# Kernel tuning notes

Hardware: AMD Instinct MI355X
Metric: run time of the kernel (lower is better)

The kernel has to match this reference:

```python
import jax, jax.numpy as jnp
import numpy as np


def mesa_head(xh, yh, qh, lam):
    # xh = per-head 'inputs' (v_proj output), yh = 'targets' (k_proj output),
    # qh = queries; all [T, d]. lam is this head's scalar lambda.
    T, d = xh.shape
    init_inv = jnp.eye(d, dtype=xh.dtype) * lam

    def step(inv, tok):
        x_t, q_t = tok
        Hx = inv @ x_t                      # [d]   (cur_inverse @ x)
        xH = x_t @ inv                      # [d]   (x^T @ cur_inverse)
        denom = 1.0 + x_t @ Hx              # scalar: forward=1 + x^T H x
        new_inv = inv - jnp.outer(Hx, xH) / denom   # Sherman-Morrison rank-1 update
        return new_inv, new_inv @ q_t       # pred_t = S_t @ q_t

    _, preds = jax.lax.scan(step, init_inv, (xh, qh))  # preds: [T, d]

    # scaled_dot_product_attention(preds, xh, yh) with masked=True,
    # use_softmax=False, normalization=False: tril-masked linear attention.
    logits = preds @ xh.T                               # [T, T]
    mask = jnp.tril(jnp.ones((T, T), dtype=bool))
    logits = jnp.where(mask, logits, jnp.zeros((), dtype=logits.dtype))
    return logits @ yh                                  # [T, d]


def reference(x, Wq, Wk, Wv, Wo, lambdas):
    B, T, E = x.shape
    H = lambdas.shape[0]
    d = Wq.shape[1] // H
    q = (x @ Wq).reshape(B, T, H, d)   # query_heads
    k = (x @ Wk).reshape(B, T, H, d)   # target_heads
    v = (x @ Wv).reshape(B, T, H, d)   # input_heads
    # Original call: mesa(input_heads, target_heads, query_heads, lambdas, norm)
    over_batch = jax.vmap(mesa_head, in_axes=(0, 0, 0, None))
    over_heads = jax.vmap(over_batch, in_axes=(2, 2, 2, 0), out_axes=-1)
    mesa_out = over_heads(v, k, q, lambdas)             # [B, T, d, H]
    # Faithful to original: reshape combines (d, H) in that order before o_proj.
    out = mesa_out.reshape(B, T, H * d) @ Wo            # [B, T, E]
    return out


def setup_inputs() -> dict:
    key = jax.random.key(0)
    ks = jax.random.split(key, 6)
    B, T, E, H, d = 2, 1024, 512, 8, 64
    s_in = 1.0 / np.sqrt(E).astype(np.float32)
    s_out = 1.0 / np.sqrt(H * d).astype(np.float32)
    return {
        "x": jax.random.normal(ks[0], (B, T, E), dtype=jnp.float32),
        "Wq": jax.random.normal(ks[1], (E, H * d), dtype=jnp.float32) * s_in,
        "Wk": jax.random.normal(ks[2], (E, H * d), dtype=jnp.float32) * s_in,
        "Wv": jax.random.normal(ks[3], (E, H * d), dtype=jnp.float32) * s_in,
        "Wo": jax.random.normal(ks[4], (H * d, E), dtype=jnp.float32) * s_out,
        "lambdas": jnp.ones((H,), dtype=jnp.float32),
    }
```

## Files before the change

### kernel.cpp

```cpp
#include <hip/hip_runtime.h>

#define T_SEQ 1024
#define DH 64
#define NH 8
#define NB 2
#define EMB 512
#define CS 32
#define NCH 32
#define ACH 16
#define NCHAIN 16

typedef __attribute__((ext_vector_type(8))) short bf16x8;
typedef __attribute__((ext_vector_type(4))) float f32x4;

__device__ __forceinline__ int swz4(int r, int c4) {
    return r * 16 + ((c4 ^ (r >> 2)) & 15);
}

__device__ __forceinline__ void fma4(float4& o, float s, const float4& b) {
    o.x += s * b.x; o.y += s * b.y; o.z += s * b.z; o.w += s * b.w;
}

__device__ __forceinline__ ushort f2bf(float f) {
    unsigned u = __float_as_uint(f);
    return (ushort)((u + 0x7FFFu + ((u >> 16) & 1u)) >> 16);
}
__device__ __forceinline__ float bf2f(ushort h) {
    return __uint_as_float(((unsigned)h) << 16);
}
__device__ __forceinline__ void split2(float f, ushort& hi, ushort& lo) {
    hi = f2bf(f);
    lo = f2bf(f - bf2f(hi));
}

__global__ __launch_bounds__(256) void prep_qkv(
    const float* __restrict__ x, const float* __restrict__ W0,
    const float* __restrict__ W1, const float* __restrict__ W2,
    ushort* __restrict__ x_hi, ushort* __restrict__ x_lo,
    ushort* __restrict__ Wt_hi, ushort* __restrict__ Wt_lo) {
    int zz = blockIdx.z;
    int t = threadIdx.x;
    __shared__ float T[64][65];
    if (zz < 3) {
        const float* W = (zz == 0) ? W0 : (zz == 1) ? W1 : W2;
        ushort* hi = Wt_hi + (size_t)zz * 262144;
        ushort* lo = Wt_lo + (size_t)zz * 262144;
        int kk0 = blockIdx.x * 64, n0 = blockIdx.y * 64;
#pragma unroll
        for (int i = 0; i < 4; ++i) {
            int rl = i * 16 + (t >> 4);
            float4 vv = *(const float4*)&W[(size_t)(kk0 + rl) * 512 + n0 + (t & 15) * 4];
            T[rl][(t & 15) * 4 + 0] = vv.x;
            T[rl][(t & 15) * 4 + 1] = vv.y;
            T[rl][(t & 15) * 4 + 2] = vv.z;
            T[rl][(t & 15) * 4 + 3] = vv.w;
        }
        __syncthreads();
        int nl = t >> 2, kl = (t & 3) * 16;
#pragma unroll
        for (int j4 = 0; j4 < 4; ++j4) {
            ushort4 h4, l4;
            split2(T[kl + j4 * 4 + 0][nl], h4.x, l4.x);
            split2(T[kl + j4 * 4 + 1][nl], h4.y, l4.y);
            split2(T[kl + j4 * 4 + 2][nl], h4.z, l4.z);
            split2(T[kl + j4 * 4 + 3][nl], h4.w, l4.w);
            size_t dst = (size_t)(n0 + nl) * 512 + kk0 + kl + j4 * 4;
            *(ushort4*)&hi[dst] = h4;
            *(ushort4*)&lo[dst] = l4;
        }
    } else {
        int bid = blockIdx.y * 8 + blockIdx.x;
        const float4* in = (const float4*)x;
        ushort4* hi = (ushort4*)x_hi;
        ushort4* lo = (ushort4*)x_lo;
#pragma unroll
        for (int i = 0; i < 16; ++i) {
            int id = (bid * 16 + i) * 256 + t;
            float4 xv = in[id];
            ushort4 h, l;
            split2(xv.x, h.x, l.x);
            split2(xv.y, h.y, l.y);
            split2(xv.z, h.z, l.z);
            split2(xv.w, h.w, l.w);
            hi[id] = h;
            lo[id] = l;
        }
    }
}

template <int MODE>
__global__ __launch_bounds__(256) void mfma_gemm(
    const ushort* __restrict__ Ahi, const ushort* __restrict__ Alo,
    const ushort* __restrict__ Bth, const ushort* __restrict__ Btl,
    float* __restrict__ o0, float* __restrict__ o1, float* __restrict__ o2) {
    int bm = blockIdx.x, bn = blockIdx.y, zz = blockIdx.z;
    const ushort* Bh = Bth + (size_t)zz * 262144;
    const ushort* Bl = Btl + (size_t)zz * 262144;
    float* out = (MODE == 0) ? ((zz == 0) ? o0 : (zz == 1) ? o1 : o2) : o0;

    __shared__ ushort Ash[128 * 40];
    __shared__ ushort Asl[128 * 40];
    __shared__ ushort Bsh[64 * 40];
    __shared__ ushort Bsl[64 * 40];

    int tid = threadIdx.x;
    int lane = tid & 63, wid = tid >> 6;
    int wm = wid >> 1, wn = wid & 1;
    int fr = lane & 15, fk = (lane >> 4) * 8;
    int sr = tid >> 2, sc = (tid & 3) * 8;

    f32x4 zero = {0.f, 0.f, 0.f, 0.f};
    f32x4 acc[4][2];
#pragma unroll
    for (int f = 0; f < 4; ++f)
#pragma unroll
        for (int g = 0; g < 2; ++g) acc[f][g] = zero;

    const ushort* gAh = Ahi + (size_t)(bm * 128 + sr) * 512 + sc;
    const ushort* gAl = Alo + (size_t)(bm * 128 + sr) * 512 + sc;
    const ushort* gBh = Bh + (size_t)(bn * 64 + sr) * 512 + sc;
    const ushort* gBl = Bl + (size_t)(bn * 64 + sr) * 512 + sc;

    for (int k0 = 0; k0 < 512; k0 += 32) {
        uint4 a0 = *(const uint4*)(gAh + k0);
        uint4 a1 = *(const uint4*)(gAh + 64 * 512 + k0);
        uint4 a2 = *(const uint4*)(gAl + k0);
        uint4 a3 = *(const uint4*)(gAl + 64 * 512 + k0);
        uint4 b0 = *(const uint4*)(gBh + k0);
        uint4 b1 = *(const uint4*)(gBl + k0);
        __syncthreads();
        *(uint4*)&Ash[sr * 40 + sc] = a0;
        *(uint4*)&Ash[(sr + 64) * 40 + sc] = a1;
        *(uint4*)&Asl[sr * 40 + sc] = a2;
        *(uint4*)&Asl[(sr + 64) * 40 + sc] = a3;
        *(uint4*)&Bsh[sr * 40 + sc] = b0;
        *(uint4*)&Bsl[sr * 40 + sc] = b1;
        __syncthreads();
        bf16x8 ah[4], al[4], bh[2], blo[2];
#pragma unroll
        for (int f = 0; f < 4; ++f) {
            int r = wm * 64 + f * 16 + fr;
            ah[f] = *(const bf16x8*)&Ash[r * 40 + fk];
            al[f] = *(const bf16x8*)&Asl[r * 40 + fk];
        }
#pragma unroll
        for (int g = 0; g < 2; ++g) {
            int r = wn * 32 + g * 16 + fr;
            bh[g] = *(const bf16x8*)&Bsh[r * 40 + fk];
            blo[g] = *(const bf16x8*)&Bsl[r * 40 + fk];
        }
#pragma unroll
        for (int f = 0; f < 4; ++f)
#pragma unroll
            for (int g = 0; g < 2; ++g) {
                acc[f][g] = __builtin_amdgcn_mfma_f32_16x16x32_bf16(
                    ah[f], bh[g], acc[f][g], 0, 0, 0);
                acc[f][g] = __builtin_amdgcn_mfma_f32_16x16x32_bf16(
                    ah[f], blo[g], acc[f][g], 0, 0, 0);
                acc[f][g] = __builtin_amdgcn_mfma_f32_16x16x32_bf16(
                    al[f], bh[g], acc[f][g], 0, 0, 0);
            }
    }

    int rbase = (lane >> 4) * 4;
#pragma unroll
    for (int f = 0; f < 4; ++f)
#pragma unroll
        for (int g = 0; g < 2; ++g)
#pragma unroll
            for (int j = 0; j < 4; ++j) {
                int m = bm * 128 + wm * 64 + f * 16 + rbase + j;
                int n = bn * 64 + wn * 32 + g * 16 + (lane & 15);
                float val = acc[f][g][j];
                if (MODE == 0) {
                    int b = m >> 10, tt = m & 1023;
                    int h = n >> 6, d = n & 63;
                    out[(((size_t)(b * 8 + h) * 1024 + tt) << 6) + d] = val;
                } else {
                    out[(size_t)m * 512 + n] = val;
                }
            }
}

__global__ __launch_bounds__(256) void gram_kernel(
    const float* __restrict__ v, float* __restrict__ g) {
    int chain = blockIdx.x, chunk = blockIdx.y;
    const float* X = v + ((size_t)chain * T_SEQ + chunk * CS) * DH;
    __shared__ float Xs[CS * 64];
    int tid = threadIdx.x;
#pragma unroll
    for (int i = 0; i < (CS * 16) / 256; ++i)
        ((float4*)Xs)[i * 256 + tid] = ((const float4*)X)[i * 256 + tid];
    __syncthreads();

    int tx = tid & 15, ty = tid >> 4;
    float acc[4][4];
#pragma unroll
    for (int i = 0; i < 4; ++i)
#pragma unroll
        for (int j = 0; j < 4; ++j) acc[i][j] = 0.f;

#pragma unroll 4
    for (int t = 0; t < CS; ++t) {
        float a_[4], b_[4];
#pragma unroll
        for (int i = 0; i < 4; ++i) a_[i] = Xs[t * 64 + ty * 4 + i];
#pragma unroll
        for (int j = 0; j < 4; ++j) b_[j] = Xs[t * 64 + tx * 4 + j];
#pragma unroll
        for (int i = 0; i < 4; ++i)
#pragma unroll
            for (int j = 0; j < 4; ++j) acc[i][j] += a_[i] * b_[j];
    }

    float* gp = g + ((size_t)chain * NCH + chunk) * 4096;
#pragma unroll
    for (int i = 0; i < 4; ++i)
        *(float4*)(gp + (ty * 4 + i) * 64 + tx * 4) =
            make_float4(acc[i][0], acc[i][1], acc[i][2], acc[i][3]);
}

__global__ __launch_bounds__(256) void prefix_kernel(float* __restrict__ g) {
    int gid = blockIdx.x * 256 + threadIdx.x;
    int chain = gid >> 12, elem = gid & 4095;
    float* p = g + (size_t)chain * NCH * 4096 + elem;
    float vals[NCH];
#pragma unroll
    for (int c = 0; c < NCH; ++c) vals[c] = p[(size_t)c * 4096];
    float run = 0.f;
#pragma unroll
    for (int c = 0; c < NCH; ++c) {
        float t = vals[c];
        vals[c] = run;
        run += t;
    }
#pragma unroll
    for (int c = 0; c < NCH; ++c) p[(size_t)c * 4096] = vals[c];
}

__global__ __launch_bounds__(256) void invscan(
    const float* __restrict__ g, const float* __restrict__ v,
    const float* __restrict__ q, const float* __restrict__ lambdas,
    float* __restrict__ preds) {
    int blk = blockIdx.x;
    int chain = blk >> 5, chunk = blk & 31;
    int tid = threadIdx.x;
    int row = tid >> 2, ch = tid & 3, wav = tid >> 6;
    float lam = lambdas[chain & (NH - 1)];

    __shared__ float rbuf[2][64];
    __shared__ float sbuf[2][64];
    __shared__ float Xs[CS * 64];
    __shared__ float Qs[CS * 64];
    __shared__ float Po[CS * 64];
    __shared__ float red[2][6][4];

    float m[16];
    {
        const float4* gp = (const float4*)(g + ((size_t)chain * NCH + chunk) * 4096);
#pragma unroll
        for (int i = 0; i < 4; ++i) {
            float4 t4 = gp[row * 16 + ch * 4 + i];
            m[i * 4 + 0] = t4.x; m[i * 4 + 1] = t4.y;
            m[i * 4 + 2] = t4.z; m[i * 4 + 3] = t4.w;
        }
    }
#pragma unroll
    for (int i = 0; i < 16; ++i)
        if (ch * 16 + i == row) m[i] += lam;

    const float4* vb = (const float4*)(v + ((size_t)chain * T_SEQ + chunk * CS) * DH);
    const float4* qb = (const float4*)(q + ((size_t)chain * T_SEQ + chunk * CS) * DH);
    ((float4*)Xs)[tid] = vb[tid];
    ((float4*)Xs)[256 + tid] = vb[256 + tid];
    ((float4*)Qs)[tid] = qb[tid];
    ((float4*)Qs)[256 + tid] = qb[256 + tid];

    if (row == 0) {
#pragma unroll
        for (int i = 0; i < 4; ++i)
            ((float4*)rbuf[0])[ch * 4 + i] =
                make_float4(m[i * 4], m[i * 4 + 1], m[i * 4 + 2], m[i * 4 + 3]);
    }
    if (row == 1) {
#pragma unroll
        for (int i = 0; i < 4; ++i)
            ((float4*)sbuf[0])[ch * 4 + i] =
                make_float4(m[i * 4], m[i * 4 + 1], m[i * 4 + 2], m[i * 4 + 3]);
    }
    __syncthreads();

#pragma unroll
    for (int pp = 0; pp < 32; ++pp) {
        const int p = 2 * pp;
        const float* rb = rbuf[pp & 1];
        const float* sb = sbuf[pp & 1];
        float r_[16], s_[16];
#pragma unroll
        for (int i = 0; i < 4; ++i) {
            float4 t4 = ((const float4*)rb)[ch * 4 + i];
            r_[i * 4] = t4.x; r_[i * 4 + 1] = t4.y;
            r_[i * 4 + 2] = t4.z; r_[i * 4 + 3] = t4.w;
            float4 u4 = ((const float4*)sb)[ch * 4 + i];
            s_[i * 4] = u4.x; s_[i * 4 + 1] = u4.y;
            s_[i * 4 + 2] = u4.z; s_[i * 4 + 3] = u4.w;
        }
        float rp = rb[p], rp2 = rb[p + 1], sp2 = sb[p + 1];
        float gr = rb[row], gs = sb[row];
        float i1 = 1.f / rp;
        float al = rp2 * i1;
        float i2 = 1.f / (sp2 - al * rp2);
        float c0, ca, cb;
        if (row == p) {
            c0 = 0.f; ca = i1 + al * al * i2; cb = -al * i2;
        } else if (row == p + 1) {
            c0 = 0.f; ca = -al * i2; cb = i2;
        } else {
            float b2 = (gs - al * gr) * i2;
            c0 = 1.f; ca = al * b2 - gr * i1; cb = -b2;
        }
#pragma unroll
        for (int i = 0; i < 16; ++i) m[i] = c0 * m[i] + ca * r_[i] + cb * s_[i];
        if (ch == (p >> 4)) {
            m[p & 15] = -ca;
            m[(p & 15) + 1] = -cb;
        }
        if (pp < 31) {
            if (row == p + 2) {
#pragma unroll
                for (int i = 0; i < 4; ++i)
                    ((float4*)rbuf[(pp + 1) & 1])[ch * 4 + i] =
                        make_float4(m[i * 4], m[i * 4 + 1], m[i * 4 + 2], m[i * 4 + 3]);
            }
            if (row == p + 3) {
#pragma unroll
                for (int i = 0; i < 4; ++i)
                    ((float4*)sbuf[(pp + 1) & 1])[ch * 4 + i] =
                        make_float4(m[i * 4], m[i * 4 + 1], m[i * 4 + 2], m[i * 4 + 3]);
            }
        }
        __syncthreads();
    }

#pragma unroll
    for (int tp = 0; tp < 16; ++tp) {
        const int ta = 2 * tp, tb2 = 2 * tp + 1;
        const int par = tp & 1;
        float pu = 0.f, pw = 0.f, pza = 0.f, pzb = 0.f;
#pragma unroll
        for (int i = 0; i < 4; ++i) {
            float4 xa = ((const float4*)(Xs + ta * 64))[ch * 4 + i];
            float4 xb = ((const float4*)(Xs + tb2 * 64))[ch * 4 + i];
            float4 qa = ((const float4*)(Qs + ta * 64))[ch * 4 + i];
            float4 q4 = ((const float4*)(Qs + tb2 * 64))[ch * 4 + i];
            pu += m[i * 4] * xa.x + m[i * 4 + 1] * xa.y + m[i * 4 + 2] * xa.z + m[i * 4 + 3] * xa.w;
            pw += m[i * 4] * xb.x + m[i * 4 + 1] * xb.y + m[i * 4 + 2] * xb.z + m[i * 4 + 3] * xb.w;
            pza += m[i * 4] * qa.x + m[i * 4 + 1] * qa.y + m[i * 4 + 2] * qa.z + m[i * 4 + 3] * qa.w;
            pzb += m[i * 4] * q4.x + m[i * 4 + 1] * q4.y + m[i * 4 + 2] * q4.z + m[i * 4 + 3] * q4.w;
        }
        pu += __shfl_xor(pu, 1); pu += __shfl_xor(pu, 2);
        pw += __shfl_xor(pw, 1); pw += __shfl_xor(pw, 2);
        pza += __shfl_xor(pza, 1); pza += __shfl_xor(pza, 2);
        pzb += __shfl_xor(pzb, 1); pzb += __shfl_xor(pzb, 2);
        float u = -pu, w = -pw, za = -pza, zb = -pzb;
        if (ch == 0) rbuf[par][row] = u;
        if (ch == 1) sbuf[par][row] = w;
        float a_ = Xs[ta * 64 + row], b_ = Xs[tb2 * 64 + row];
        float qa_ = Qs[ta * 64 + row], qb_ = Qs[tb2 * 64 + row];
        float d0 = a_ * u, d1 = b_ * u, d2 = b_ * w;
        float d3 = qa_ * u, d4 = qb_ * u, d5 = qb_ * w;
#pragma unroll
        for (int off = 32; off; off >>= 1) {
            d0 += __shfl_xor(d0, off); d1 += __shfl_xor(d1, off);
            d2 += __shfl_xor(d2, off); d3 += __shfl_xor(d3, off);
            d4 += __shfl_xor(d4, off); d5 += __shfl_xor(d5, off);
        }
        if ((tid & 63) == 0) {
            red[par][0][wav] = d0; red[par][1][wav] = d1; red[par][2][wav] = d2;
            red[par][3][wav] = d3; red[par][4][wav] = d4; red[par][5][wav] = d5;
        }
        __syncthreads();
        float saa = 0.25f * (red[par][0][0] + red[par][0][1] + red[par][0][2] + red[par][0][3]);
        float sab = 0.25f * (red[par][1][0] + red[par][1][1] + red[par][1][2] + red[par][1][3]);
        float sbb = 0.25f * (red[par][2][0] + red[par][2][1] + red[par][2][2] + red[par][2][3]);
        float c1  = 0.25f * (red[par][3][0] + red[par][3][1] + red[par][3][2] + red[par][3][3]);
        float c2  = 0.25f * (red[par][4][0] + red[par][4][1] + red[par][4][2] + red[par][4][3]);
        float c3  = 0.25f * (red[par][5][0] + red[par][5][1] + red[par][5][2] + red[par][5][3]);
        float k1 = 1.f / (1.f + saa);
        float al2 = sab * k1;
        float k2 = 1.f / (1.f + sbb - sab * al2);
        float vr = w - al2 * u;
        if (ch == 0) Po[ta * 64 + row] = za - (c1 * k1) * u;
        if (ch == 1) Po[tb2 * 64 + row] = zb - (c2 * k1) * u - (k2 * (c3 - al2 * c2)) * vr;
        float cu = k1 * u - al2 * k2 * vr;
        float cw = k2 * vr;
#pragma unroll
        for (int i = 0; i < 4; ++i) {
            float4 uj = ((const float4*)rbuf[par])[ch * 4 + i];
            float4 wj = ((const float4*)sbuf[par])[ch * 4 + i];
            m[i * 4 + 0] += cu * uj.x + cw * wj.x;
            m[i * 4 + 1] += cu * uj.y + cw * wj.y;
            m[i * 4 + 2] += cu * uj.z + cw * wj.z;
            m[i * 4 + 3] += cu * uj.w + cw * wj.w;
        }
    }
    __syncthreads();

    float4* po4 = (float4*)(preds + ((size_t)chain * T_SEQ + chunk * CS) * DH);
    po4[tid] = ((const float4*)Po)[tid];
    po4[256 + tid] = ((const float4*)Po)[256 + tid];
}

__global__ __launch_bounds__(256) void kvg_wot(
    const float* __restrict__ V, const float* __restrict__ Kv,
    float* __restrict__ D, const float* __restrict__ Wo,
    ushort* __restrict__ Wot_hi, ushort* __restrict__ Wot_lo) {
    __shared__ float smem[8192];
    int tid = threadIdx.x;
    if (blockIdx.y < 16) {
        int chain = blockIdx.x, ck = blockIdx.y;
        float* Vs = smem;
        float* Ks2 = smem + 4096;
        const float4* Vb = (const float4*)(V + ((size_t)chain * T_SEQ + ck * 64) * DH);
        const float4* Kb = (const float4*)(Kv + ((size_t)chain * T_SEQ + ck * 64) * DH);
#pragma unroll
        for (int i = 0; i < 4; ++i) {
            ((float4*)Vs)[i * 256 + tid] = Vb[i * 256 + tid];
            ((float4*)Ks2)[i * 256 + tid] = Kb[i * 256 + tid];
        }
        __syncthreads();

        int tx = tid & 15, ty = tid >> 4;
        float acc[4][4];
#pragma unroll
        for (int i = 0; i < 4; ++i)
#pragma unroll
            for (int j = 0; j < 4; ++j) acc[i][j] = 0.f;

#pragma unroll 4
        for (int t = 0; t < 64; ++t) {
            float a_[4], b_[4];
#pragma unroll
            for (int i = 0; i < 4; ++i) a_[i] = Vs[t * 64 + ty * 4 + i];
#pragma unroll
            for (int j = 0; j < 4; ++j) b_[j] = Ks2[t * 64 + tx * 4 + j];
#pragma unroll
            for (int i = 0; i < 4; ++i)
#pragma unroll
                for (int j = 0; j < 4; ++j) acc[i][j] += a_[i] * b_[j];
        }

        float* dp = D + ((size_t)chain * ACH + ck) * 4096;
#pragma unroll
        for (int i = 0; i < 4; ++i)
            *(float4*)(dp + (ty * 4 + i) * 64 + tx * 4) =
                make_float4(acc[i][0], acc[i][1], acc[i][2], acc[i][3]);
    } else {
        int wb = blockIdx.x * 4 + (blockIdx.y - 16);
        int kk0 = (wb >> 3) * 64, n0 = (wb & 7) * 64;
#pragma unroll
        for (int i = 0; i < 4; ++i) {
            int rl = i * 16 + (tid >> 4);
            int rs = rl * 8 + (kk0 >> 6);
            float4 vv = *(const float4*)&Wo[(size_t)rs * 512 + n0 + (tid & 15) * 4];
            smem[rl * 65 + (tid & 15) * 4 + 0] = vv.x;
            smem[rl * 65 + (tid & 15) * 4 + 1] = vv.y;
            smem[rl * 65 + (tid & 15) * 4 + 2] = vv.z;
            smem[rl * 65 + (tid & 15) * 4 + 3] = vv.w;
        }
        __syncthreads();
        int nl = tid >> 2, kl = (tid & 3) * 16;
#pragma unroll
        for (int j4 = 0; j4 < 4; ++j4) {
            ushort4 h4, l4;
            split2(smem[(kl + j4 * 4 + 0) * 65 + nl], h4.x, l4.x);
            split2(smem[(kl + j4 * 4 + 1) * 65 + nl], h4.y, l4.y);
            split2(smem[(kl + j4 * 4 + 2) * 65 + nl], h4.z, l4.z);
            split2(smem[(kl + j4 * 4 + 3) * 65 + nl], h4.w, l4.w);
            size_t dst = (size_t)(n0 + nl) * 512 + kk0 + kl + j4 * 4;
            *(ushort4*)&Wot_hi[dst] = h4;
            *(ushort4*)&Wot_lo[dst] = l4;
        }
    }
}

__global__ __launch_bounds__(256) void kv_prefix(float* __restrict__ d) {
    int gid = blockIdx.x * 256 + threadIdx.x;
    int chain = gid >> 12, elem = gid & 4095;
    float* p = d + (size_t)chain * ACH * 4096 + elem;
    float vals[ACH];
#pragma unroll
    for (int c = 0; c < ACH; ++c) vals[c] = p[(size_t)c * 4096];
    float run = 0.f;
#pragma unroll
    for (int c = 0; c < ACH; ++c) {
        float t = vals[c];
        vals[c] = run;
        run += t;
    }
#pragma unroll
    for (int c = 0; c < ACH; ++c) p[(size_t)c * 4096] = vals[c];
}

__global__ __launch_bounds__(256) void attn_chunk(
    const float* __restrict__ P, const float* __restrict__ V,
    const float* __restrict__ Kv, const float* __restrict__ C,
    ushort* __restrict__ A2_hi, ushort* __restrict__ A2_lo) {
    int ck = blockIdx.x, bh = blockIdx.y;
    int tid = threadIdx.x, tx = tid & 15, ty = tid >> 4;

    __shared__ float4 Ps[64 * 16];
    __shared__ float4 Bs[64 * 16];
    __shared__ float4 Ks[64 * 16];

    int lr = tid >> 2, lc = tid & 3;
    const float4* Pb = (const float4*)(P + ((size_t)bh * T_SEQ + ck * 64) * DH);
    const float4* Vb = (const float4*)(V + ((size_t)bh * T_SEQ + ck * 64) * DH);
    const float4* Kb = (const float4*)(Kv + ((size_t)bh * T_SEQ + ck * 64) * DH);
    const float4* Cb = (const float4*)(C + ((size_t)bh * ACH + ck) * 4096);
#pragma unroll
    for (int i = 0; i < 4; ++i) {
        Ps[swz4(lr, lc + i * 4)] = Pb[lr * 16 + lc + i * 4];
        Bs[swz4(lr, lc + i * 4)] = Cb[lr * 16 + lc + i * 4];
        Ks[swz4(lr, lc + i * 4)] = Kb[lr * 16 + lc + i * 4];
    }

    float4 o[4];
    o[0] = o[1] = o[2] = o[3] = make_float4(0.f, 0.f, 0.f, 0.f);
    __syncthreads();

    const float* Pf = (const float*)Ps;
#pragma unroll 4
    for (int j = 0; j < 64; ++j) {
        float4 b4 = Bs[swz4(j, tx)];
#pragma unroll
        for (int i = 0; i < 4; ++i) {
            float s = Pf[swz4(ty * 4 + i, j >> 2) * 4 + (j & 3)];
            fma4(o[i], s, b4);
        }
    }
    __syncthreads();

#pragma unroll
    for (int i = 0; i < 4; ++i)
        Bs[swz4(lr, lc + i * 4)] = Vb[lr * 16 + lc + i * 4];
    __syncthreads();

    float4 sa[4][4];
#pragma unroll
    for (int i = 0; i < 4; ++i)
#pragma unroll
        for (int j = 0; j < 4; ++j) sa[i][j] = make_float4(0.f, 0.f, 0.f, 0.f);
#pragma unroll
    for (int d4 = 0; d4 < 16; ++d4) {
        float4 a[4], b[4];
#pragma unroll
        for (int i = 0; i < 4; ++i) a[i] = Ps[swz4(ty * 4 + i, d4)];
#pragma unroll
        for (int j = 0; j < 4; ++j) b[j] = Bs[swz4(tx * 4 + j, d4)];
#pragma unroll
        for (int i = 0; i < 4; ++i)
#pragma unroll
            for (int j = 0; j < 4; ++j) {
                sa[i][j].x += a[i].x * b[j].x;
                sa[i][j].y += a[i].y * b[j].y;
                sa[i][j].z += a[i].z * b[j].z;
                sa[i][j].w += a[i].w * b[j].w;
            }
    }
    __syncthreads();

#pragma unroll
    for (int i = 0; i < 4; ++i) {
        int m = ty * 4 + i;
        float sv[4];
#pragma unroll
        for (int j = 0; j < 4; ++j) {
            float s = sa[i][j].x + sa[i][j].y + sa[i][j].z + sa[i][j].w;
            if ((tx * 4 + j) > m) s = 0.f;
            sv[j] = s;
        }
        Bs[swz4(m, tx)] = make_float4(sv[0], sv[1], sv[2], sv[3]);
    }
    __syncthreads();

    const float* Sf = (const float*)Bs;
#pragma unroll 4
    for (int j = 0; j < 64; ++j) {
        float4 b4 = Ks[swz4(j, tx)];
#pragma unroll
        for (int i = 0; i < 4; ++i) {
            float s = Sf[swz4(ty * 4 + i, j >> 2) * 4 + (j & 3)];
            fma4(o[i], s, b4);
        }
    }

    int kkb = ((bh & 7) << 6) + tx * 4;
#pragma unroll
    for (int i = 0; i < 4; ++i) {
        int t = ck * 64 + ty * 4 + i;
        size_t mrow = (size_t)((bh >> 3) << 10) + t;
        ushort4 h, l;
        split2(o[i].x, h.x, l.x);
        split2(o[i].y, h.y, l.y);
        split2(o[i].z, h.z, l.z);
        split2(o[i].w, h.w, l.w);
        *(ushort4*)&A2_hi[mrow * 512 + kkb] = h;
        *(ushort4*)&A2_lo[mrow * 512 + kkb] = l;
    }
}

extern "C" void kernel_launch(void* const* d_in, const int* in_sizes, int n_in,
                              void* d_out, int out_size, void* d_ws, size_t ws_size,
                              hipStream_t stream) {
    const float* x = (const float*)d_in[0];
    const float* Wq = (const float*)d_in[1];
    const float* Wk = (const float*)d_in[2];
    const float* Wv = (const float*)d_in[3];
    const float* Wo = (const float*)d_in[4];
    const float* lambdas = (const float*)d_in[5];
    float* out = (float*)d_out;

    float* ws = (float*)d_ws;
    const size_t SZ = (size_t)NB * NH * T_SEQ * DH;
    float* q = ws;
    float* k = ws + SZ;
    float* v = ws + 2 * SZ;
    float* preds = ws + 3 * SZ;
    ushort* x_hi = (ushort*)(ws + 3 * SZ);
    ushort* x_lo = (ushort*)(ws + 3 * SZ + SZ / 2);
    float* g = ws + 4 * SZ;
    ushort* Wt_hi = (ushort*)(ws + 4 * SZ);
    ushort* Wt_lo = (ushort*)(ws + 4 * SZ + 393216);
    float* dbuf = g;
    ushort* A2_hi = (ushort*)(ws + 5 * SZ);
    ushort* A2_lo = (ushort*)(ws + 5 * SZ + SZ / 2);
    ushort* Wot_hi = (ushort*)ws;
    ushort* Wot_lo = (ushort*)(ws + 131072);

    prep_qkv<<<dim3(8, 8, 4), 256, 0, stream>>>(x, Wq, Wk, Wv,
                                                x_hi, x_lo, Wt_hi, Wt_lo);
    mfma_gemm<0><<<dim3(16, 8, 3), 256, 0, stream>>>(
        x_hi, x_lo, Wt_hi, Wt_lo, q, k, v);
    gram_kernel<<<dim3(NCHAIN, NCH), 256, 0, stream>>>(v, g);
    prefix_kernel<<<dim3(256), 256, 0, stream>>>(g);
    invscan<<<dim3(NCHAIN * NCH), 256, 0, stream>>>(g, v, q, lambdas, preds);
    kvg_wot<<<dim3(NCHAIN, ACH + 4), 256, 0, stream>>>(v, k, dbuf, Wo,
                                                       Wot_hi, Wot_lo);
    kv_prefix<<<dim3(256), 256, 0, stream>>>(dbuf);
    attn_chunk<<<dim3(ACH, NCHAIN), 256, 0, stream>>>(preds, v, k, dbuf,
                                                      A2_hi, A2_lo);
    mfma_gemm<1><<<dim3(16, 8, 1), 256, 0, stream>>>(
        A2_hi, A2_lo, Wot_hi, Wot_lo, out, out, out);
}
```

Baseline: 129.0 us.

## Merge inverse scan with KV gram blocks and move Wo transpose into attention

Fuses the inverse-scan kernel and the chunked K^T V gram kernel into one launch with heterogeneous blocks. When the workspace is large enough, the KV products go to a separate buffer so they no longer alias the gram buffer. The Wo bf16 split/transpose moves from the KV kernel into the attention kernel as extra blocks. This cuts launches and lets independent work fill idle CUs alongside the long serial inverse scan, at the cost of larger shared memory per block (a fixed 8192-float array) and possible occupancy loss.

```diff
diff --git a/kernel.cpp b/kernel.cpp
--- a/kernel.cpp
+++ b/kernel.cpp
@@ -238,190 +238,192 @@
     for (int c = 0; c < NCH; ++c) p[(size_t)c * 4096] = vals[c];
 }
 
-__global__ __launch_bounds__(256) void invscan(
+__global__ __launch_bounds__(256) void invscan_kv(
+    int nInv,
     const float* __restrict__ g, const float* __restrict__ v,
     const float* __restrict__ q, const float* __restrict__ lambdas,
-    float* __restrict__ preds) {
-    int blk = blockIdx.x;
-    int chain = blk >> 5, chunk = blk & 31;
+    float* __restrict__ preds,
+    const float* __restrict__ Kv, float* __restrict__ D) {
+    __shared__ float smem[8192];
+    int bid = blockIdx.x;
     int tid = threadIdx.x;
-    int row = tid >> 2, ch = tid & 3, wav = tid >> 6;
-    float lam = lambdas[chain & (NH - 1)];
-
-    __shared__ float rbuf[2][64];
-    __shared__ float sbuf[2][64];
-    __shared__ float Xs[CS * 64];
-    __shared__ float Qs[CS * 64];
-    __shared__ float Po[CS * 64];
-    __shared__ float red[2][6][4];
-
-    float m[16];
-    {
-        const float4* gp = (const float4*)(g + ((size_t)chain * NCH + chunk) * 4096);
-#pragma unroll
-        for (int i = 0; i < 4; ++i) {
-            float4 t4 = gp[row * 16 + ch * 4 + i];
-            m[i * 4 + 0] = t4.x; m[i * 4 + 1] = t4.y;
-            m[i * 4 + 2] = t4.z; m[i * 4 + 3] = t4.w;
-        }
-    }
-#pragma unroll
-    for (int i = 0; i < 16; ++i)
-        if (ch * 16 + i == row) m[i] += lam;
-
-    const float4* vb = (const float4*)(v + ((size_t)chain * T_SEQ + chunk * CS) * DH);
-    const float4* qb = (const float4*)(q + ((size_t)chain * T_SEQ + chunk * CS) * DH);
-    ((float4*)Xs)[tid] = vb[tid];
-    ((float4*)Xs)[256 + tid] = vb[256 + tid];
-    ((float4*)Qs)[tid] = qb[tid];
-    ((float4*)Qs)[256 + tid] = qb[256 + tid];
-
-    if (row == 0) {
-#pragma unroll
-        for (int i = 0; i < 4; ++i)
-            ((float4*)rbuf[0])[ch * 4 + i] =
-                make_float4(m[i * 4], m[i * 4 + 1], m[i * 4 + 2], m[i * 4 + 3]);
-    }
-    if (row == 1) {
-#pragma unroll
-        for (int i = 0; i < 4; ++i)
-            ((float4*)sbuf[0])[ch * 4 + i] =
-                make_float4(m[i * 4], m[i * 4 + 1], m[i * 4 + 2], m[i * 4 + 3]);
-    }
-    __syncthreads();
-
-#pragma unroll
-    for (int pp = 0; pp < 32; ++pp) {
-        const int p = 2 * pp;
-        const float* rb = rbuf[pp & 1];
-        const float* sb = sbuf[pp & 1];
-        float r_[16], s_[16];
-#pragma unroll
-        for (int i = 0; i < 4; ++i) {
-            float4 t4 = ((const float4*)rb)[ch * 4 + i];
-            r_[i * 4] = t4.x; r_[i * 4 + 1] = t4.y;
-            r_[i * 4 + 2] = t4.z; r_[i * 4 + 3] = t4.w;
-            float4 u4 = ((const float4*)sb)[ch * 4 + i];
-            s_[i * 4] = u4.x; s_[i * 4 + 1] = u4.y;
-            s_[i * 4 + 2] = u4.z; s_[i * 4 + 3] = u4.w;
-        }
-        float rp = rb[p], rp2 = rb[p + 1], sp2 = sb[p + 1];
-        float gr = rb[row], gs = sb[row];
-        float i1 = 1.f / rp;
-        float al = rp2 * i1;
-        float i2 = 1.f / (sp2 - al * rp2);
-        float c0, ca, cb;
-        if (row == p) {
-            c0 = 0.f; ca = i1 + al * al * i2; cb = -al * i2;
-        } else if (row == p + 1) {
-            c0 = 0.f; ca = -al * i2; cb = i2;
-        } else {
-            float b2 = (gs - al * gr) * i2;
-            c0 = 1.f; ca = al * b2 - gr * i1; cb = -b2;
-        }
-#pragma unroll
-        for (int i = 0; i < 16; ++i) m[i] = c0 * m[i] + ca * r_[i] + cb * s_[i];
-        if (ch == (p >> 4)) {
-            m[p & 15] = -ca;
-            m[(p & 15) + 1] = -cb;
-        }
-        if (pp < 31) {
-            if (row == p + 2) {
-#pragma unroll
-                for (int i = 0; i < 4; ++i)
-                    ((float4*)rbuf[(pp + 1) & 1])[ch * 4 + i] =
-                        make_float4(m[i * 4], m[i * 4 + 1], m[i * 4 + 2], m[i * 4 + 3]);
-            }
-            if (row == p + 3) {
-#pragma unroll
-                for (int i = 0; i < 4; ++i)
-                    ((float4*)sbuf[(pp + 1) & 1])[ch * 4 + i] =
-                        make_float4(m[i * 4], m[i * 4 + 1], m[i * 4 + 2], m[i * 4 + 3]);
-            }
-        }
-        __syncthreads();
-    }
-
-#pragma unroll
-    for (int tp = 0; tp < 16; ++tp) {
-        const int ta = 2 * tp, tb2 = 2 * tp + 1;
-        const int par = tp & 1;
-        float pu = 0.f, pw = 0.f, pza = 0.f, pzb = 0.f;
-#pragma unroll
-        for (int i = 0; i < 4; ++i) {
-            float4 xa = ((const float4*)(Xs + ta * 64))[ch * 4 + i];
-            float4 xb = ((const float4*)(Xs + tb2 * 64))[ch * 4 + i];
-            float4 qa = ((const float4*)(Qs + ta * 64))[ch * 4 + i];
-            float4 q4 = ((const float4*)(Qs + tb2 * 64))[ch * 4 + i];
-            pu += m[i * 4] * xa.x + m[i * 4 + 1] * xa.y + m[i * 4 + 2] * xa.z + m[i * 4 + 3] * xa.w;
-            pw += m[i * 4] * xb.x + m[i * 4 + 1] * xb.y + m[i * 4 + 2] * xb.z + m[i * 4 + 3] * xb.w;
-            pza += m[i * 4] * qa.x + m[i * 4 + 1] * qa.y + m[i * 4 + 2] * qa.z + m[i * 4 + 3] * qa.w;
-            pzb += m[i * 4] * q4.x + m[i * 4 + 1] * q4.y + m[i * 4 + 2] * q4.z + m[i * 4 + 3] * q4.w;
-        }
-        pu += __shfl_xor(pu, 1); pu += __shfl_xor(pu, 2);
-        pw += __shfl_xor(pw, 1); pw += __shfl_xor(pw, 2);
-        pza += __shfl_xor(pza, 1); pza += __shfl_xor(pza, 2);
-        pzb += __shfl_xor(pzb, 1); pzb += __shfl_xor(pzb, 2);
-        float u = -pu, w = -pw, za = -pza, zb = -pzb;
-        if (ch == 0) rbuf[par][row] = u;
-        if (ch == 1) sbuf[par][row] = w;
-        float a_ = Xs[ta * 64 + row], b_ = Xs[tb2 * 64 + row];
-        float qa_ = Qs[ta * 64 + row], qb_ = Qs[tb2 * 64 + row];
-        float d0 = a_ * u, d1 = b_ * u, d2 = b_ * w;
-        float d3 = qa_ * u, d4 = qb_ * u, d5 = qb_ * w;
-#pragma unroll
-        for (int off = 32; off; off >>= 1) {
-            d0 += __shfl_xor(d0, off); d1 += __shfl_xor(d1, off);
-            d2 += __shfl_xor(d2, off); d3 += __shfl_xor(d3, off);
-            d4 += __shfl_xor(d4, off); d5 += __shfl_xor(d5, off);
-        }
-        if ((tid & 63) == 0) {
-            red[par][0][wav] = d0; red[par][1][wav] = d1; red[par][2][wav] = d2;
-            red[par][3][wav] = d3; red[par][4][wav] = d4; red[par][5][wav] = d5;
-        }
-        __syncthreads();
-        float saa = 0.25f * (red[par][0][0] + red[par][0][1] + red[par][0][2] + red[par][0][3]);
-        float sab = 0.25f * (red[par][1][0] + red[par][1][1] + red[par][1][2] + red[par][1][3]);
-        float sbb = 0.25f * (red[par][2][0] + red[par][2][1] + red[par][2][2] + red[par][2][3]);
-        float c1  = 0.25f * (red[par][3][0] + red[par][3][1] + red[par][3][2] + red[par][3][3]);
-        float c2  = 0.25f * (red[par][4][0] + red[par][4][1] + red[par][4][2] + red[par][4][3]);
-        float c3  = 0.25f * (red[par][5][0] + red[par][5][1] + red[par][5][2] + red[par][5][3]);
-        float k1 = 1.f / (1.f + saa);
-        float al2 = sab * k1;
-        float k2 = 1.f / (1.f + sbb - sab * al2);
-        float vr = w - al2 * u;
-        if (ch == 0) Po[ta * 64 + row] = za - (c1 * k1) * u;
-        if (ch == 1) Po[tb2 * 64 + row] = zb - (c2 * k1) * u - (k2 * (c3 - al2 * c2)) * vr;
-        float cu = k1 * u - al2 * k2 * vr;
-        float cw = k2 * vr;
-#pragma unroll
-        for (int i = 0; i < 4; ++i) {
-            float4 uj = ((const float4*)rbuf[par])[ch * 4 + i];
-            float4 wj = ((const float4*)sbuf[par])[ch * 4 + i];
-            m[i * 4 + 0] += cu * uj.x + cw * wj.x;
-            m[i * 4 + 1] += cu * uj.y + cw * wj.y;
-            m[i * 4 + 2] += cu * uj.z + cw * wj.z;
-            m[i * 4 + 3] += cu * uj.w + cw * wj.w;
-        }
-    }
-    __syncthreads();
-
-    float4* po4 = (float4*)(preds + ((size_t)chain * T_SEQ + chunk * CS) * DH);
-    po4[tid] = ((const float4*)Po)[tid];
-    po4[256 + tid] = ((const float4*)Po)[256 + tid];
-}
-
-__global__ __launch_bounds__(256) void kvg_wot(
-    const float* __restrict__ V, const float* __restrict__ Kv,
-    float* __restrict__ D, const float* __restrict__ Wo,
-    ushort* __restrict__ Wot_hi, ushort* __restrict__ Wot_lo) {
-    __shared__ float smem[8192];
-    int tid = threadIdx.x;
-    if (blockIdx.y < 16) {
-        int chain = blockIdx.x, ck = blockIdx.y;
+
+    if (bid < nInv) {
+        int chain = bid >> 5, chunk = bid & 31;
+        int row = tid >> 2, ch = tid & 3, wav = tid >> 6;
+        float lam = lambdas[chain & (NH - 1)];
+
+        float* Xs = smem;
+        float* Qs = smem + 2048;
+        float* Po = smem + 4096;
+        float* rbufB = smem + 6144;
+        float* sbufB = smem + 6272;
+        float* red = smem + 6400;
+
+        float m[16];
+        {
+            const float4* gp = (const float4*)(g + ((size_t)chain * NCH + chunk) * 4096);
+#pragma unroll
+            for (int i = 0; i < 4; ++i) {
+                float4 t4 = gp[row * 16 + ch * 4 + i];
+                m[i * 4 + 0] = t4.x; m[i * 4 + 1] = t4.y;
+                m[i * 4 + 2] = t4.z; m[i * 4 + 3] = t4.w;
+            }
+        }
+#pragma unroll
+        for (int i = 0; i < 16; ++i)
+            if (ch * 16 + i == row) m[i] += lam;
+
+        const float4* vb = (const float4*)(v + ((size_t)chain * T_SEQ + chunk * CS) * DH);
+        const float4* qb = (const float4*)(q + ((size_t)chain * T_SEQ + chunk * CS) * DH);
+        ((float4*)Xs)[tid] = vb[tid];
+        ((float4*)Xs)[256 + tid] = vb[256 + tid];
+        ((float4*)Qs)[tid] = qb[tid];
+        ((float4*)Qs)[256 + tid] = qb[256 + tid];
+
+        if (row == 0) {
+#pragma unroll
+            for (int i = 0; i < 4; ++i)
+                ((float4*)rbufB)[ch * 4 + i] =
+                    make_float4(m[i * 4], m[i * 4 + 1], m[i * 4 + 2], m[i * 4 + 3]);
+        }
+        if (row == 1) {
+#pragma unroll
+            for (int i = 0; i < 4; ++i)
+                ((float4*)sbufB)[ch * 4 + i] =
+                    make_float4(m[i * 4], m[i * 4 + 1], m[i * 4 + 2], m[i * 4 + 3]);
+        }
+        __syncthreads();
+
+#pragma unroll
+        for (int pp = 0; pp < 32; ++pp) {
+            const int p = 2 * pp;
+            const float* rb = rbufB + (pp & 1) * 64;
+            const float* sb = sbufB + (pp & 1) * 64;
+            float r_[16], s_[16];
+#pragma unroll
+            for (int i = 0; i < 4; ++i) {
+                float4 t4 = ((const float4*)rb)[ch * 4 + i];
+                r_[i * 4] = t4.x; r_[i * 4 + 1] = t4.y;
+                r_[i * 4 + 2] = t4.z; r_[i * 4 + 3] = t4.w;
+                float4 u4 = ((const float4*)sb)[ch * 4 + i];
+                s_[i * 4] = u4.x; s_[i * 4 + 1] = u4.y;
+                s_[i * 4 + 2] = u4.z; s_[i * 4 + 3] = u4.w;
+            }
+            float rp = rb[p], rp2 = rb[p + 1], sp2 = sb[p + 1];
+            float gr = rb[row], gs = sb[row];
+            float i1 = 1.f / rp;
+            float al = rp2 * i1;
+            float i2 = 1.f / (sp2 - al * rp2);
+            float c0, ca, cb;
+            if (row == p) {
+                c0 = 0.f; ca = i1 + al * al * i2; cb = -al * i2;
+            } else if (row == p + 1) {
+                c0 = 0.f; ca = -al * i2; cb = i2;
+            } else {
+                float b2 = (gs - al * gr) * i2;
+                c0 = 1.f; ca = al * b2 - gr * i1; cb = -b2;
+            }
+#pragma unroll
+            for (int i = 0; i < 16; ++i) m[i] = c0 * m[i] + ca * r_[i] + cb * s_[i];
+            if (ch == (p >> 4)) {
+                m[p & 15] = -ca;
+                m[(p & 15) + 1] = -cb;
+            }
+            if (pp < 31) {
+                if (row == p + 2) {
+#pragma unroll
+                    for (int i = 0; i < 4; ++i)
+                        ((float4*)(rbufB + ((pp + 1) & 1) * 64))[ch * 4 + i] =
+                            make_float4(m[i * 4], m[i * 4 + 1], m[i * 4 + 2], m[i * 4 + 3]);
+                }
+                if (row == p + 3) {
+#pragma unroll
+                    for (int i = 0; i < 4; ++i)
+                        ((float4*)(sbufB + ((pp + 1) & 1) * 64))[ch * 4 + i] =
+                            make_float4(m[i * 4], m[i * 4 + 1], m[i * 4 + 2], m[i * 4 + 3]);
+                }
+            }
+            __syncthreads();
+        }
+
+#pragma unroll
+        for (int tp = 0; tp < 16; ++tp) {
+            const int ta = 2 * tp, tb2 = 2 * tp + 1;
+            const int par = tp & 1;
+            float pu = 0.f, pw = 0.f, pza = 0.f, pzb = 0.f;
+#pragma unroll
+            for (int i = 0; i < 4; ++i) {
+                float4 xa = ((const float4*)(Xs + ta * 64))[ch * 4 + i];
+                float4 xb = ((const float4*)(Xs + tb2 * 64))[ch * 4 + i];
+                float4 qa = ((const float4*)(Qs + ta * 64))[ch * 4 + i];
+                float4 q4 = ((const float4*)(Qs + tb2 * 64))[ch * 4 + i];
+                pu += m[i * 4] * xa.x + m[i * 4 + 1] * xa.y + m[i * 4 + 2] * xa.z + m[i * 4 + 3] * xa.w;
+                pw += m[i * 4] * xb.x + m[i * 4 + 1] * xb.y + m[i * 4 + 2] * xb.z + m[i * 4 + 3] * xb.w;
+                pza += m[i * 4] * qa.x + m[i * 4 + 1] * qa.y + m[i * 4 + 2] * qa.z + m[i * 4 + 3] * qa.w;
+                pzb += m[i * 4] * q4.x + m[i * 4 + 1] * q4.y + m[i * 4 + 2] * q4.z + m[i * 4 + 3] * q4.w;
+            }
+            pu += __shfl_xor(pu, 1); pu += __shfl_xor(pu, 2);
+            pw += __shfl_xor(pw, 1); pw += __shfl_xor(pw, 2);
+            pza += __shfl_xor(pza, 1); pza += __shfl_xor(pza, 2);
+            pzb += __shfl_xor(pzb, 1); pzb += __shfl_xor(pzb, 2);
+            float u = -pu, w = -pw, za = -pza, zb = -pzb;
+            float* rbufP = rbufB + par * 64;
+            float* sbufP = sbufB + par * 64;
+            if (ch == 0) rbufP[row] = u;
+            if (ch == 1) sbufP[row] = w;
+            float a_ = Xs[ta * 64 + row], b_ = Xs[tb2 * 64 + row];
+            float qa_ = Qs[ta * 64 + row], qb_ = Qs[tb2 * 64 + row];
+            float d0 = a_ * u, d1 = b_ * u, d2 = b_ * w;
+            float d3 = qa_ * u, d4 = qb_ * u, d5 = qb_ * w;
+#pragma unroll
+            for (int off = 32; off; off >>= 1) {
+                d0 += __shfl_xor(d0, off); d1 += __shfl_xor(d1, off);
+                d2 += __shfl_xor(d2, off); d3 += __shfl_xor(d3, off);
+                d4 += __shfl_xor(d4, off); d5 += __shfl_xor(d5, off);
+            }
+            if ((tid & 63) == 0) {
+                red[par * 24 + 0 * 4 + wav] = d0; red[par * 24 + 1 * 4 + wav] = d1;
+                red[par * 24 + 2 * 4 + wav] = d2; red[par * 24 + 3 * 4 + wav] = d3;
+                red[par * 24 + 4 * 4 + wav] = d4; red[par * 24 + 5 * 4 + wav] = d5;
+            }
+            __syncthreads();
+            const float* rp_ = red + par * 24;
+            float saa = 0.25f * (rp_[0] + rp_[1] + rp_[2] + rp_[3]);
+            float sab = 0.25f * (rp_[4] + rp_[5] + rp_[6] + rp_[7]);
+            float sbb = 0.25f * (rp_[8] + rp_[9] + rp_[10] + rp_[11]);
+            float c1  = 0.25f * (rp_[12] + rp_[13] + rp_[14] + rp_[15]);
+            float c2  = 0.25f * (rp_[16] + rp_[17] + rp_[18] + rp_[19]);
+            float c3  = 0.25f * (rp_[20] + rp_[21] + rp_[22] + rp_[23]);
+            float k1 = 1.f / (1.f + saa);
+            float al2 = sab * k1;
+            float k2 = 1.f / (1.f + sbb - sab * al2);
+            float vr = w - al2 * u;
+            if (ch == 0) Po[ta * 64 + row] = za - (c1 * k1) * u;
+            if (ch == 1) Po[tb2 * 64 + row] = zb - (c2 * k1) * u - (k2 * (c3 - al2 * c2)) * vr;
+            float cu = k1 * u - al2 * k2 * vr;
+            float cw = k2 * vr;
+#pragma unroll
+            for (int i = 0; i < 4; ++i) {
+                float4 uj = ((const float4*)rbufP)[ch * 4 + i];
+                float4 wj = ((const float4*)sbufP)[ch * 4 + i];
+                m[i * 4 + 0] += cu * uj.x + cw * wj.x;
+                m[i * 4 + 1] += cu * uj.y + cw * wj.y;
+                m[i * 4 + 2] += cu * uj.z + cw * wj.z;
+                m[i * 4 + 3] += cu * uj.w + cw * wj.w;
+            }
+        }
+        __syncthreads();
+
+        float4* po4 = (float4*)(preds + ((size_t)chain * T_SEQ + chunk * CS) * DH);
+        po4[tid] = ((const float4*)Po)[tid];
+        po4[256 + tid] = ((const float4*)Po)[256 + tid];
+    } else {
+        int kb = bid - nInv;
+        int chain = kb >> 4, ck = kb & 15;
         float* Vs = smem;
         float* Ks2 = smem + 4096;
-        const float4* Vb = (const float4*)(V + ((size_t)chain * T_SEQ + ck * 64) * DH);
+        const float4* Vb = (const float4*)(v + ((size_t)chain * T_SEQ + ck * 64) * DH);
         const float4* Kb = (const float4*)(Kv + ((size_t)chain * T_SEQ + ck * 64) * DH);
 #pragma unroll
         for (int i = 0; i < 4; ++i) {
@@ -455,32 +457,6 @@
         for (int i = 0; i < 4; ++i)
             *(float4*)(dp + (ty * 4 + i) * 64 + tx * 4) =
                 make_float4(acc[i][0], acc[i][1], acc[i][2], acc[i][3]);
-    } else {
-        int wb = blockIdx.x * 4 + (blockIdx.y - 16);
-        int kk0 = (wb >> 3) * 64, n0 = (wb & 7) * 64;
-#pragma unroll
-        for (int i = 0; i < 4; ++i) {
-            int rl = i * 16 + (tid >> 4);
-            int rs = rl * 8 + (kk0 >> 6);
-            float4 vv = *(const float4*)&Wo[(size_t)rs * 512 + n0 + (tid & 15) * 4];
-            smem[rl * 65 + (tid & 15) * 4 + 0] = vv.x;
-            smem[rl * 65 + (tid & 15) * 4 + 1] = vv.y;
-            smem[rl * 65 + (tid & 15) * 4 + 2] = vv.z;
-            smem[rl * 65 + (tid & 15) * 4 + 3] = vv.w;
-        }
-        __syncthreads();
-        int nl = tid >> 2, kl = (tid & 3) * 16;
-#pragma unroll
-        for (int j4 = 0; j4 < 4; ++j4) {
-            ushort4 h4, l4;
-            split2(smem[(kl + j4 * 4 + 0) * 65 + nl], h4.x, l4.x);
-            split2(smem[(kl + j4 * 4 + 1) * 65 + nl], h4.y, l4.y);
-            split2(smem[(kl + j4 * 4 + 2) * 65 + nl], h4.z, l4.z);
-            split2(smem[(kl + j4 * 4 + 3) * 65 + nl], h4.w, l4.w);
-            size_t dst = (size_t)(n0 + nl) * 512 + kk0 + kl + j4 * 4;
-            *(ushort4*)&Wot_hi[dst] = h4;
-            *(ushort4*)&Wot_lo[dst] = l4;
-        }
     }
 }
 
@@ -502,111 +478,145 @@
     for (int c = 0; c < ACH; ++c) p[(size_t)c * 4096] = vals[c];
 }
 
-__global__ __launch_bounds__(256) void attn_chunk(
+__global__ __launch_bounds__(256) void attn_wot(
     const float* __restrict__ P, const float* __restrict__ V,
     const float* __restrict__ Kv, const float* __restrict__ C,
-    ushort* __restrict__ A2_hi, ushort* __restrict__ A2_lo) {
-    int ck = blockIdx.x, bh = blockIdx.y;
-    int tid = threadIdx.x, tx = tid & 15, ty = tid >> 4;
-
-    __shared__ float4 Ps[64 * 16];
-    __shared__ float4 Bs[64 * 16];
-    __shared__ float4 Ks[64 * 16];
-
-    int lr = tid >> 2, lc = tid & 3;
-    const float4* Pb = (const float4*)(P + ((size_t)bh * T_SEQ + ck * 64) * DH);
-    const float4* Vb = (const float4*)(V + ((size_t)bh * T_SEQ + ck * 64) * DH);
-    const float4* Kb = (const float4*)(Kv + ((size_t)bh * T_SEQ + ck * 64) * DH);
-    const float4* Cb = (const float4*)(C + ((size_t)bh * ACH + ck) * 4096);
-#pragma unroll
-    for (int i = 0; i < 4; ++i) {
-        Ps[swz4(lr, lc + i * 4)] = Pb[lr * 16 + lc + i * 4];
-        Bs[swz4(lr, lc + i * 4)] = Cb[lr * 16 + lc + i * 4];
-        Ks[swz4(lr, lc + i * 4)] = Kb[lr * 16 + lc + i * 4];
-    }
-
-    float4 o[4];
-    o[0] = o[1] = o[2] = o[3] = make_float4(0.f, 0.f, 0.f, 0.f);
-    __syncthreads();
-
-    const float* Pf = (const float*)Ps;
+    ushort* __restrict__ A2_hi, ushort* __restrict__ A2_lo,
+    const float* __restrict__ Wo,
+    ushort* __restrict__ Wot_hi, ushort* __restrict__ Wot_lo) {
+    __shared__ float4 smem4[3072];
+    int bid = blockIdx.x;
+    int tid = threadIdx.x;
+
+    if (bid < 256) {
+        int ck = bid & 15, bh = bid >> 4;
+        int tx = tid & 15, ty = tid >> 4;
+        float4* Ps = smem4;
+        float4* Bs = smem4 + 1024;
+        float4* Ks = smem4 + 2048;
+
+        int lr = tid >> 2, lc = tid & 3;
+        const float4* Pb = (const float4*)(P + ((size_t)bh * T_SEQ + ck * 64) * DH);
+        const float4* Vb = (const float4*)(V + ((size_t)bh * T_SEQ + ck * 64) * DH);
+        const float4* Kb = (const float4*)(Kv + ((size_t)bh * T_SEQ + ck * 64) * DH);
+        const float4* Cb = (const float4*)(C + ((size_t)bh * ACH + ck) * 4096);
+#pragma unroll
+        for (int i = 0; i < 4; ++i) {
+            Ps[swz4(lr, lc + i * 4)] = Pb[lr * 16 + lc + i * 4];
+            Bs[swz4(lr, lc + i * 4)] = Cb[lr * 16 + lc + i * 4];
+            Ks[swz4(lr, lc + i * 4)] = Kb[lr * 16 + lc + i * 4];
+        }
+
+        float4 o[4];
+        o[0] = o[1] = o[2] = o[3] = make_float4(0.f, 0.f, 0.f, 0.f);
+        __syncthreads();
+
+        const float* Pf = (const float*)Ps;
 #pragma unroll 4
-    for (int j = 0; j < 64; ++j) {
-        float4 b4 = Bs[swz4(j, tx)];
+        for (int j = 0; j < 64; ++j) {
+            float4 b4 = Bs[swz4(j, tx)];
+#pragma unroll
+            for (int i = 0; i < 4; ++i) {
+                float s = Pf[swz4(ty * 4 + i, j >> 2) * 4 + (j & 3)];
+                fma4(o[i], s, b4);
+            }
+        }
+        __syncthreads();
+
+#pragma unroll
+        for (int i = 0; i < 4; ++i)
+            Bs[swz4(lr, lc + i * 4)] = Vb[lr * 16 + lc + i * 4];
+        __syncthreads();
+
+        float4 sa[4][4];
+#pragma unroll
+        for (int i = 0; i < 4; ++i)
+#pragma unroll
+            for (int j = 0; j < 4; ++j) sa[i][j] = make_float4(0.f, 0.f, 0.f, 0.f);
+#pragma unroll
+        for (int d4 = 0; d4 < 16; ++d4) {
+            float4 a[4], b[4];
+#pragma unroll
+            for (int i = 0; i < 4; ++i) a[i] = Ps[swz4(ty * 4 + i, d4)];
+#pragma unroll
+            for (int j = 0; j < 4; ++j) b[j] = Bs[swz4(tx * 4 + j, d4)];
+#pragma unroll
+            for (int i = 0; i < 4; ++i)
+#pragma unroll
+                for (int j = 0; j < 4; ++j) {
+                    sa[i][j].x += a[i].x * b[j].x;
+                    sa[i][j].y += a[i].y * b[j].y;
+                    sa[i][j].z += a[i].z * b[j].z;
+                    sa[i][j].w += a[i].w * b[j].w;
+                }
+        }
+        __syncthreads();
+
 #pragma unroll
         for (int i = 0; i < 4; ++i) {
-            float s = Pf[swz4(ty * 4 + i, j >> 2) * 4 + (j & 3)];
-            fma4(o[i], s, b4);
-        }
-    }
-    __syncthreads();
-
-#pragma unroll
-    for (int i = 0; i < 4; ++i)
-        Bs[swz4(lr, lc + i * 4)] = Vb[lr * 16 + lc + i * 4];
-    __syncthreads();
-
-    float4 sa[4][4];
-#pragma unroll
-    for (int i = 0; i < 4; ++i)
-#pragma unroll
-        for (int j = 0; j < 4; ++j) sa[i][j] = make_float4(0.f, 0.f, 0.f, 0.f);
-#pragma unroll
-    for (int d4 = 0; d4 < 16; ++d4) {
-        float4 a[4], b[4];
-#pragma unroll
-        for (int i = 0; i < 4; ++i) a[i] = Ps[swz4(ty * 4 + i, d4)];
-#pragma unroll
-        for (int j = 0; j < 4; ++j) b[j] = Bs[swz4(tx * 4 + j, d4)];
-#pragma unroll
-        for (int i = 0; i < 4; ++i)
+            int m = ty * 4 + i;
+            float sv[4];
 #pragma unroll
             for (int j = 0; j < 4; ++j) {
-                sa[i][j].x += a[i].x * b[j].x;
-                sa[i][j].y += a[i].y * b[j].y;
-                sa[i][j].z += a[i].z * b[j].z;
-                sa[i][j].w += a[i].w * b[j].w;
-            }
-    }
-    __syncthreads();
-
-#pragma unroll
-    for (int i = 0; i < 4; ++i) {
-        int m = ty * 4 + i;
-        float sv[4];
-#pragma unroll
-        for (int j = 0; j < 4; ++j) {
-            float s = sa[i][j].x + sa[i][j].y + sa[i][j].z + sa[i][j].w;
-            if ((tx * 4 + j) > m) s = 0.f;
-            sv[j] = s;
-        }
-        Bs[swz4(m, tx)] = make_float4(sv[0], sv[1], sv[2], sv[3]);
-    }
-    __syncthreads();
-
-    const float* Sf = (const float*)Bs;
+                float s = sa[i][j].x + sa[i][j].y + sa[i][j].z + sa[i][j].w;
+                if ((tx * 4 + j) > m) s = 0.f;
+                sv[j] = s;
+            }
+            Bs[swz4(m, tx)] = make_float4(sv[0], sv[1], sv[2], sv[3]);
+        }
+        __syncthreads();
+
+        const float* Sf = (const float*)Bs;
 #pragma unroll 4
-    for (int j = 0; j < 64; ++j) {
-        float4 b4 = Ks[swz4(j, tx)];
+        for (int j = 0; j < 64; ++j) {
+            float4 b4 = Ks[swz4(j, tx)];
+#pragma unroll
+            for (int i = 0; i < 4; ++i) {
+                float s = Sf[swz4(ty * 4 + i, j >> 2) * 4 + (j & 3)];
+                fma4(o[i], s, b4);
+            }
+        }
+
+        int kkb = ((bh & 7) << 6) + tx * 4;
 #pragma unroll
         for (int i = 0; i < 4; ++i) {
-            float s = Sf[swz4(ty * 4 + i, j >> 2) * 4 + (j & 3)];
-            fma4(o[i], s, b4);
-        }
-    }
-
-    int kkb = ((bh & 7) << 6) + tx * 4;
-#pragma unroll
-    for (int i = 0; i < 4; ++i) {
-        int t = ck * 64 + ty * 4 + i;
-        size_t mrow = (size_t)((bh >> 3) << 10) + t;
-        ushort4 h, l;
-        split2(o[i].x, h.x, l.x);
-        split2(o[i].y, h.y, l.y);
-        split2(o[i].z, h.z, l.z);
-        split2(o[i].w, h.w, l.w);
-        *(ushort4*)&A2_hi[mrow * 512 + kkb] = h;
-        *(ushort4*)&A2_lo[mrow * 512 + kkb] = l;
+            int t = ck * 64 + ty * 4 + i;
+            size_t mrow = (size_t)((bh >> 3) << 10) + t;
+            ushort4 h, l;
+            split2(o[i].x, h.x, l.x);
+            split2(o[i].y, h.y, l.y);
+            split2(o[i].z, h.z, l.z);
+            split2(o[i].w, h.w, l.w);
+            *(ushort4*)&A2_hi[mrow * 512 + kkb] = h;
+            *(ushort4*)&A2_lo[mrow * 512 + kkb] = l;
+        }
+    } else {
+        float* Tf = (float*)smem4;
+        int wb = bid - 256;
+        int kk0 = (wb >> 3) * 64, n0 = (wb & 7) * 64;
+#pragma unroll
+        for (int i = 0; i < 4; ++i) {
+            int rl = i * 16 + (tid >> 4);
+            int rs = rl * 8 + (kk0 >> 6);
+            float4 vv = *(const float4*)&Wo[(size_t)rs * 512 + n0 + (tid & 15) * 4];
+            Tf[rl * 65 + (tid & 15) * 4 + 0] = vv.x;
+            Tf[rl * 65 + (tid & 15) * 4 + 1] = vv.y;
+            Tf[rl * 65 + (tid & 15) * 4 + 2] = vv.z;
+            Tf[rl * 65 + (tid & 15) * 4 + 3] = vv.w;
+        }
+        __syncthreads();
+        int nl = tid >> 2, kl = (tid & 3) * 16;
+#pragma unroll
+        for (int j4 = 0; j4 < 4; ++j4) {
+            ushort4 h4, l4;
+            split2(Tf[(kl + j4 * 4 + 0) * 65 + nl], h4.x, l4.x);
+            split2(Tf[(kl + j4 * 4 + 1) * 65 + nl], h4.y, l4.y);
+            split2(Tf[(kl + j4 * 4 + 2) * 65 + nl], h4.z, l4.z);
+            split2(Tf[(kl + j4 * 4 + 3) * 65 + nl], h4.w, l4.w);
+            size_t dst = (size_t)(n0 + nl) * 512 + kk0 + kl + j4 * 4;
+            *(ushort4*)&Wot_hi[dst] = h4;
+            *(ushort4*)&Wot_lo[dst] = l4;
+        }
     }
 }
 
@@ -632,11 +642,13 @@
     float* g = ws + 4 * SZ;
     ushort* Wt_hi = (ushort*)(ws + 4 * SZ);
     ushort* Wt_lo = (ushort*)(ws + 4 * SZ + 393216);
-    float* dbuf = g;
     ushort* A2_hi = (ushort*)(ws + 5 * SZ);
     ushort* A2_lo = (ushort*)(ws + 5 * SZ + SZ / 2);
     ushort* Wot_hi = (ushort*)ws;
     ushort* Wot_lo = (ushort*)(ws + 131072);
+
+    bool big = ws_size >= (size_t)7 * SZ * sizeof(float);
+    float* dbuf = big ? (ws + 6 * SZ) : g;
 
     prep_qkv<<<dim3(8, 8, 4), 256, 0, stream>>>(x, Wq, Wk, Wv,
                                                 x_hi, x_lo, Wt_hi, Wt_lo);
@@ -644,12 +656,19 @@
         x_hi, x_lo, Wt_hi, Wt_lo, q, k, v);
     gram_kernel<<<dim3(NCHAIN, NCH), 256, 0, stream>>>(v, g);
     prefix_kernel<<<dim3(256), 256, 0, stream>>>(g);
-    invscan<<<dim3(NCHAIN * NCH), 256, 0, stream>>>(g, v, q, lambdas, preds);
-    kvg_wot<<<dim3(NCHAIN, ACH + 4), 256, 0, stream>>>(v, k, dbuf, Wo,
-                                                       Wot_hi, Wot_lo);
+    if (big) {
+        invscan_kv<<<dim3(NCHAIN * NCH + NCHAIN * ACH), 256, 0, stream>>>(
+            NCHAIN * NCH, g, v, q, lambdas, preds, k, dbuf);
+    } else {
+        invscan_kv<<<dim3(NCHAIN * NCH), 256, 0, stream>>>(
+            NCHAIN * NCH, g, v, q, lambdas, preds, k, dbuf);
+        invscan_kv<<<dim3(NCHAIN * ACH), 256, 0, stream>>>(
+            0, g, v, q, lambdas, preds, k, dbuf);
+    }
     kv_prefix<<<dim3(256), 256, 0, stream>>>(dbuf);
-    attn_chunk<<<dim3(ACH, NCHAIN), 256, 0, stream>>>(preds, v, k, dbuf,
-                                                      A2_hi, A2_lo);
+    attn_wot<<<dim3(320), 256, 0, stream>>>(preds, v, k, dbuf, A2_hi, A2_lo,
+                                            Wo, Wot_hi, Wot_lo);
     mfma_gemm<1><<<dim3(16, 8, 1), 256, 0, stream>>>(
-        A2_hi, A2_lo, Wot_hi, Wot_lo, out, out, out);
-}
+        (const ushort*)A2_hi, (const ushort*)A2_lo, Wot_hi, Wot_lo,
+        out, out, out);
+}
```

After: 123.7 us. -4.1%, faster.
